# Performance work log

Measured on AMD Instinct MI355X. Metric: run time of the kernel, lower is better.

The kernel has to match this reference:

```python
import jax, jax.numpy as jnp
import numpy as np

NUM_HEADS = 8
ALPHA = 4.0  # spikingjelly sigmoid surrogate default

@jax.custom_vjp
def spike(x):
    return (x >= 0.0).astype(x.dtype)

def _spike_fwd(x):
    return spike(x), x

def _spike_bwd(x, g):
    s = jax.nn.sigmoid(ALPHA * x)
    return (g * ALPHA * s * (1.0 - s),)

spike.defvjp(_spike_fwd, _spike_bwd)

def lif(x, v_th=1.0, tau=2.0):
    # multi-step LIF over leading T dim; v_reset=0, hard reset, detach_reset
    def step(v, xt):
        h = v + (xt - v) / tau
        s = spike(h - v_th)
        v_new = h * (1.0 - jax.lax.stop_gradient(s))
        return v_new, s
    _, out = jax.lax.scan(step, jnp.zeros_like(x[0]), x)
    return out

def bn(x, gamma, beta, mean, var, eps=1e-5):
    # inference BatchNorm2d on (N,C,H,W)
    inv = gamma / jnp.sqrt(var + eps)
    return x * inv[None, :, None, None] + (beta - mean * inv)[None, :, None, None]

def conv1x1(x, w, b=None):
    # x: (N,C,H,W), w: (O,C)
    y = jnp.einsum('nchw,oc->nohw', x, w)
    if b is not None:
        y = y + b[None, :, None, None]
    return y

def setup_inputs() -> dict:
    key = jax.random.key(0)
    ks = jax.random.split(key, 20)
    T, B, C, H, W = 4, 32, 384, 14, 14
    d = {
        'x': jax.random.normal(ks[0], (T, B, C, H, W), jnp.float32),
        'q_w': jax.random.normal(ks[1], (C, C), jnp.float32) * (1.0 / np.sqrt(C)),
        'q_gamma': jax.random.uniform(ks[2], (C,), jnp.float32),
        'q_beta': jax.random.normal(ks[3], (C,), jnp.float32) * 0.1,
        'q_mean': jax.random.normal(ks[4], (C,), jnp.float32) * 0.1,
        'q_var': jax.random.uniform(ks[5], (C,), jnp.float32) + 0.5,
        'k_w': jax.random.normal(ks[6], (C, C), jnp.float32) * (1.0 / np.sqrt(C)),
        'k_gamma': jax.random.uniform(ks[7], (C,), jnp.float32),
        'k_beta': jax.random.normal(ks[8], (C,), jnp.float32) * 0.1,
        'k_mean': jax.random.normal(ks[9], (C,), jnp.float32) * 0.1,
        'k_var': jax.random.uniform(ks[10], (C,), jnp.float32) + 0.5,
        'proj_w': jax.random.normal(ks[11], (C, C), jnp.float32) * (1.0 / np.sqrt(C)),
        'proj_b': jax.random.normal(ks[12], (C,), jnp.float32) * 0.1,
        'proj_gamma': jax.random.uniform(ks[13], (C,), jnp.float32),
        'proj_beta': jax.random.normal(ks[14], (C,), jnp.float32) * 0.1,
        'proj_mean': jax.random.normal(ks[15], (C,), jnp.float32) * 0.1,
        'proj_var': jax.random.uniform(ks[16], (C,), jnp.float32) + 0.5,
    }
    return d

def reference(x, q_w, q_gamma, q_beta, q_mean, q_var,
              k_w, k_gamma, k_beta, k_mean, k_var,
              proj_w, proj_b, proj_gamma, proj_beta, proj_mean, proj_var):
    T, B, C, H, W = x.shape
    dh = C // NUM_HEADS
    xf = x.reshape(T * B, C, H, W)
    # Q branch: conv1x1 -> BN -> multistep LIF
    q = bn(conv1x1(xf, q_w), q_gamma, q_beta, q_mean, q_var).reshape(T, B, C, H, W)
    q = lif(q).reshape(T, B, NUM_HEADS, dh, H, W)
    # K branch
    k = bn(conv1x1(xf, k_w), k_gamma, k_beta, k_mean, k_var).reshape(T, B, C, H, W)
    k = lif(k).reshape(T, B, NUM_HEADS, dh, H, W)
    # sum-pool attention: sum q over head feature dim, spike it, gate k
    qs = jnp.sum(q, axis=3, keepdims=True)          # (T,B,heads,1,H,W)
    attn = lif(qs, v_th=0.5)
    y = (attn * k).reshape(T * B, C, H, W)
    # output projection: conv1x1(+bias) -> BN -> LIF
    y = bn(conv1x1(y, proj_w, proj_b), proj_gamma, proj_beta, proj_mean, proj_var)
    y = lif(y.reshape(T, B, C, H, W))
    return y
```

## Files before the change

kernel.cpp:

```cpp
#include <hip/hip_runtime.h>

#define C_DIM 384
#define S_DIM 196
#define CS_   (C_DIM * S_DIM)
#define BCS   (32 * CS_)
#define NELEM (128 * CS_)
#define NBS   6272

typedef _Float16 half8  __attribute__((ext_vector_type(8)));
typedef float    floatx4 __attribute__((ext_vector_type(4)));

__device__ __forceinline__ void gl_lds16(const _Float16* g, _Float16* l) {
    __builtin_amdgcn_global_load_lds(
        (const __attribute__((address_space(1))) unsigned int*)g,
        (__attribute__((address_space(3))) unsigned int*)l, 16, 0, 0);
}

__global__ __launch_bounds__(256)
void prep(const float* __restrict__ X,
          const float* __restrict__ qw, const float* __restrict__ kw,
          const float* __restrict__ pw,
          const float* qg, const float* qb, const float* qm, const float* qv,
          const float* kg, const float* kb, const float* km, const float* kv,
          const float* pg, const float* pb, const float* pm, const float* pv,
          _Float16* __restrict__ X0, _Float16* __restrict__ X1,
          _Float16* __restrict__ Wq0, _Float16* __restrict__ Wq1,
          _Float16* __restrict__ Wp0, _Float16* __restrict__ Wp1,
          float2* __restrict__ invshQ, float2* __restrict__ invshP)
{
    __shared__ float tile[32][201];
    const int bid = blockIdx.x;
    const int t   = threadIdx.x;
    if (bid < 1536) {
        const int tb = bid / 12, cch = bid % 12;
        const int tt = tb >> 5, b = tb & 31;
        const int c0 = cch * 32;
        for (int idx = t; idx < 32 * S_DIM; idx += 256) {
            const int cc = idx / S_DIM, s = idx - cc * S_DIM;
            tile[cc][s] = X[(size_t)tb * CS_ + (c0 + cc) * S_DIM + s];
        }
        __syncthreads();
        for (int idx = t; idx < 32 * S_DIM; idx += 256) {
            const int s = idx >> 5, cc = idx & 31;
            const float v = tile[cc][s];
            const _Float16 h0 = (_Float16)v;
            const size_t off = ((size_t)(b * S_DIM + s) * 4 + tt) * C_DIM + c0 + cc;
            X0[off] = h0;
            X1[off] = (_Float16)((v - (float)h0) * 4096.0f);
        }
    } else {
        const int i = (bid - 1536) * 256 + t;
        const int NQ = 768 * C_DIM;
        if (i < NQ) {
            const int o = i / C_DIM, c = i - o * C_DIM;
            const float v = (o < 384) ? qw[o * C_DIM + c] : kw[(o - 384) * C_DIM + c];
            const _Float16 h0 = (_Float16)v;
            Wq0[i] = h0;
            Wq1[i] = (_Float16)((v - (float)h0) * 4096.0f);
        } else if (i < NQ + C_DIM * C_DIM) {
            const int j = i - NQ;
            const float v = pw[j];
            const _Float16 h0 = (_Float16)v;
            Wp0[j] = h0;
            Wp1[j] = (_Float16)((v - (float)h0) * 4096.0f);
        }
        if (i < 768) {
            float g, b2, m, vv;
            if (i < 384) { g = qg[i]; b2 = qb[i]; m = qm[i]; vv = qv[i]; }
            else         { g = kg[i-384]; b2 = kb[i-384]; m = km[i-384]; vv = kv[i-384]; }
            const float inv = g / sqrtf(vv + 1e-5f);
            invshQ[i] = make_float2(inv, b2 - m * inv);
        } else if (i < 1152) {
            const int j = i - 768;
            const float inv = pg[j] / sqrtf(pv[j] + 1e-5f);
            invshP[j] = make_float2(inv, pb[j] - pm[j] * inv);
        }
    }
}

__global__ __launch_bounds__(256, 3)
void qk_mfma(const _Float16* __restrict__ A0, const _Float16* __restrict__ A1,
             const _Float16* __restrict__ B0, const _Float16* __restrict__ B1,
             const float2* __restrict__ invsh,
             unsigned char* __restrict__ spkQ, unsigned char* __restrict__ spkK)
{
    __shared__ __align__(16) _Float16 As0[128 * 32];
    __shared__ __align__(16) _Float16 As1[128 * 32];
    __shared__ __align__(16) _Float16 Bs0[128 * 32];
    __shared__ __align__(16) _Float16 Bs1[128 * 32];

    const int t    = threadIdx.x;
    const int wave = t >> 6, lane = t & 63;
    const int o0 = blockIdx.x * 128;
    const int m0 = blockIdx.y * 128;

    const int wR   = wave * 32;
    const int sRow = lane >> 2;
    const int sCol = (((lane & 3) ^ ((sRow >> 1) & 3))) << 3;

    const int lo = lane & 15, quad = lane >> 4;
    const int oq = (wave >> 1) * 64, mq = (wave & 1) * 64;
    const int rdC = (quad ^ ((lo >> 1) & 3)) << 3;

    floatx4 acc[4][4];
    #pragma unroll
    for (int i = 0; i < 4; ++i)
        #pragma unroll
        for (int j = 0; j < 4; ++j) acc[i][j] = (floatx4)0.0f;

    for (int kt = 0; kt < 12; ++kt) {
        __syncthreads();
        const int kb = kt * 32;
        #pragma unroll
        for (int u = 0; u < 2; ++u) {
            const int R = wR + u * 16;
            const size_t ga = (size_t)(o0 + R + sRow) * C_DIM + kb + sCol;
            const size_t gb = (size_t)(m0 + R + sRow) * C_DIM + kb + sCol;
            gl_lds16(A0 + ga, &As0[R * 32]);
            gl_lds16(A1 + ga, &As1[R * 32]);
            gl_lds16(B0 + gb, &Bs0[R * 32]);
            gl_lds16(B1 + gb, &Bs1[R * 32]);
        }
        __syncthreads();

        half8 w0F[4], w1F[4], x0F[4], x1F[4];
        #pragma unroll
        for (int j = 0; j < 4; ++j) {
            const int ra = (oq + j * 16 + lo) * 32 + rdC;
            w0F[j] = *(const half8*)&As0[ra];
            w1F[j] = *(const half8*)&As1[ra];
        }
        #pragma unroll
        for (int i = 0; i < 4; ++i) {
            const int rb = (mq + i * 16 + lo) * 32 + rdC;
            x0F[i] = *(const half8*)&Bs0[rb];
            x1F[i] = *(const half8*)&Bs1[rb];
        }
        #pragma unroll
        for (int i = 0; i < 4; ++i) {
            const half8 xS = x0F[i] * (_Float16)4096.0f;
            #pragma unroll
            for (int j = 0; j < 4; ++j) {
                acc[i][j] = __builtin_amdgcn_mfma_f32_16x16x32_f16(
                    x0F[i], w1F[j], acc[i][j], 0, 0, 0);
                acc[i][j] = __builtin_amdgcn_mfma_f32_16x16x32_f16(
                    x1F[i], w0F[j], acc[i][j], 0, 0, 0);
                acc[i][j] = __builtin_amdgcn_mfma_f32_16x16x32_f16(
                    xS,     w0F[j], acc[i][j], 0, 0, 0);
            }
        }
    }

    #pragma unroll
    for (int j = 0; j < 4; ++j) {
        const int o = o0 + oq + j * 16 + lo;
        const float2 is = invsh[o];
        const float inv = is.x * (1.0f / 4096.0f);
        const float sh  = is.y;
        unsigned char* base = (o < 384) ? spkQ : spkK;
        const int orow = (o < 384) ? o : o - 384;
        #pragma unroll
        for (int i = 0; i < 4; ++i) {
            const int bs = ((m0 + mq + i * 16) >> 2) + quad;
            float v = 0.0f; int bits = 0;
            #pragma unroll
            for (int r = 0; r < 4; ++r) {
                const float xv = acc[i][j][r] * inv + sh;
                const float h = v + (xv - v) * 0.5f;
                const int sp = (h >= 1.0f);
                v = sp ? 0.0f : h;
                bits |= sp << r;
            }
            base[(size_t)bs * C_DIM + orow] = (unsigned char)bits;
        }
    }
}

__global__ __launch_bounds__(256, 3)
void proj_mfma(const _Float16* __restrict__ A0, const _Float16* __restrict__ A1,
               const unsigned char* __restrict__ spkQ,
               const unsigned char* __restrict__ spkK,
               const float* __restrict__ bias, const float2* __restrict__ invsh,
               float* __restrict__ out)
{
    __shared__ __align__(16) _Float16 smem[3 * 128 * 32];
    __shared__ unsigned char attnL[256];
    _Float16* As0 = smem;
    _Float16* As1 = smem + 4096;
    _Float16* Bs0 = smem + 8192;

    const int t    = threadIdx.x;
    const int wave = t >> 6, lane = t & 63;
    const int o0 = blockIdx.x * 128;
    const int m0 = blockIdx.y * 128;

    const int wR   = wave * 32;
    const int sRow = lane >> 2;
    const int sCol = (((lane & 3) ^ ((sRow >> 1) & 3))) << 3;
    const int gC8  = (lane & 3) << 3;
    const int pC8  = sCol;

    const int lo = lane & 15, quad = lane >> 4;
    const int oq = (wave >> 1) * 64, mq = (wave & 1) * 64;
    const int rdC = (quad ^ ((lo >> 1) & 3)) << 3;

    const int bs0g   = m0 >> 2;
    const int bsl[2] = { (wR +  0 + sRow) >> 2, (wR + 16 + sRow) >> 2 };
    const int ttL    = (wR + sRow) & 3;

    {
        const int bsl_a = t >> 3, head = t & 7;
        const unsigned long long* p = (const unsigned long long*)
            (spkQ + (size_t)(bs0g + bsl_a) * C_DIM + head * 48);
        int qs[4] = {0, 0, 0, 0};
        #pragma unroll
        for (int u = 0; u < 6; ++u) {
            const unsigned long long v = p[u];
            qs[0] += __popcll(v & 0x0101010101010101ull);
            qs[1] += __popcll(v & 0x0202020202020202ull);
            qs[2] += __popcll(v & 0x0404040404040404ull);
            qs[3] += __popcll(v & 0x0808080808080808ull);
        }
        float va = 0.0f; int bits = 0;
        #pragma unroll
        for (int tt = 0; tt < 4; ++tt) {
            const float h = va + ((float)qs[tt] - va) * 0.5f;
            const int a = (h >= 0.5f);
            va = a ? 0.0f : h;
            bits |= a << tt;
        }
        attnL[t] = (unsigned char)bits;
    }
    __syncthreads();

    floatx4 acc[4][4];
    #pragma unroll
    for (int i = 0; i < 4; ++i)
        #pragma unroll
        for (int j = 0; j < 4; ++j) acc[i][j] = (floatx4)0.0f;

    unsigned long long rk[2];
    int rab[2];
    {
        const int head0 = gC8 / 48;
        #pragma unroll
        for (int u = 0; u < 2; ++u) {
            rk[u]  = *(const unsigned long long*)
                     (spkK + (size_t)(bs0g + bsl[u]) * C_DIM + gC8);
            rab[u] = (attnL[bsl[u] * 8 + head0] >> ttL) & 1;
        }
    }

    for (int kt = 0; kt < 12; ++kt) {
        __syncthreads();
        const int kb = kt * 32;
        #pragma unroll
        for (int u = 0; u < 2; ++u) {
            const int R = wR + u * 16;
            half8 bv;
            #pragma unroll
            for (int e = 0; e < 8; ++e)
                bv[e] = (_Float16)(float)((int)(rk[u] >> (8 * e + ttL)) & rab[u] & 1);
            *(half8*)&Bs0[(R + sRow) * 32 + pC8] = bv;
            const size_t ga = (size_t)(o0 + R + sRow) * C_DIM + kb + sCol;
            gl_lds16(A0 + ga, &As0[R * 32]);
            gl_lds16(A1 + ga, &As1[R * 32]);
        }
        if (kt < 11) {
            const int kb2  = (kt + 1) * 32;
            const int head = (kb2 + gC8) / 48;
            #pragma unroll
            for (int u = 0; u < 2; ++u) {
                rk[u]  = *(const unsigned long long*)
                         (spkK + (size_t)(bs0g + bsl[u]) * C_DIM + kb2 + gC8);
                rab[u] = (attnL[bsl[u] * 8 + head] >> ttL) & 1;
            }
        }
        __syncthreads();

        half8 w0F[4], w1F[4], yF[4];
        #pragma unroll
        for (int j = 0; j < 4; ++j) {
            const int ra = (oq + j * 16 + lo) * 32 + rdC;
            w0F[j] = *(const half8*)&As0[ra];
            w1F[j] = *(const half8*)&As1[ra];
        }
        #pragma unroll
        for (int i = 0; i < 4; ++i)
            yF[i] = *(const half8*)&Bs0[(mq + i * 16 + lo) * 32 + rdC];

        #pragma unroll
        for (int j = 0; j < 4; ++j) {
            const half8 wS = w0F[j] * (_Float16)4096.0f;
            #pragma unroll
            for (int i = 0; i < 4; ++i) {
                acc[i][j] = __builtin_amdgcn_mfma_f32_16x16x32_f16(
                    yF[i], w1F[j], acc[i][j], 0, 0, 0);
                acc[i][j] = __builtin_amdgcn_mfma_f32_16x16x32_f16(
                    yF[i], wS,     acc[i][j], 0, 0, 0);
            }
        }
    }

    int bits[4][4];
    #pragma unroll
    for (int j = 0; j < 4; ++j) {
        const int o = o0 + oq + j * 16 + lo;
        const float2 is = invsh[o];
        const float bv = bias[o];
        #pragma unroll
        for (int i = 0; i < 4; ++i) {
            float v = 0.0f; int bt = 0;
            #pragma unroll
            for (int r = 0; r < 4; ++r) {
                const float p = acc[i][j][r] * (1.0f / 4096.0f);
                const float z = (p + bv) * is.x + is.y;
                const float h = v + (z - v) * 0.5f;
                const int sp = (h >= 1.0f);
                v = sp ? 0.0f : h;
                bt |= sp << r;
            }
            bits[i][j] = bt;
        }
    }

    float* tile = (float*)smem;
    for (int r = 0; r < 4; ++r) {
        __syncthreads();
        #pragma unroll
        for (int j = 0; j < 4; ++j)
            #pragma unroll
            for (int i = 0; i < 4; ++i)
                tile[(oq + j * 16 + lo) * 33 + (mq >> 2) + i * 4 + quad] =
                    ((bits[i][j] >> r) & 1) ? 1.0f : 0.0f;
        __syncthreads();
        #pragma unroll
        for (int it = 0; it < 4; ++it) {
            const int idx = it * 256 + t;
            const int o   = idx >> 3;
            const int ch  = idx & 7;
            const int bsg = bs0g + ch * 4;
            const int b   = bsg / S_DIM;
            const int s   = bsg - b * S_DIM;
            float4 vv;
            vv.x = tile[o * 33 + ch * 4 + 0];
            vv.y = tile[o * 33 + ch * 4 + 1];
            vv.z = tile[o * 33 + ch * 4 + 2];
            vv.w = tile[o * 33 + ch * 4 + 3];
            *(float4*)(out + (size_t)r * BCS + (size_t)b * CS_
                           + (size_t)(o0 + o) * S_DIM + s) = vv;
        }
    }
}

extern "C" void kernel_launch(void* const* d_in, const int* in_sizes, int n_in,
                              void* d_out, int out_size, void* d_ws, size_t ws_size,
                              hipStream_t stream)
{
    const float* x          = (const float*)d_in[0];
    const float* q_w        = (const float*)d_in[1];
    const float* q_gamma    = (const float*)d_in[2];
    const float* q_beta     = (const float*)d_in[3];
    const float* q_mean     = (const float*)d_in[4];
    const float* q_var      = (const float*)d_in[5];
    const float* k_w        = (const float*)d_in[6];
    const float* k_gamma    = (const float*)d_in[7];
    const float* k_beta     = (const float*)d_in[8];
    const float* k_mean     = (const float*)d_in[9];
    const float* k_var      = (const float*)d_in[10];
    const float* proj_w     = (const float*)d_in[11];
    const float* proj_b     = (const float*)d_in[12];
    const float* proj_gamma = (const float*)d_in[13];
    const float* proj_beta  = (const float*)d_in[14];
    const float* proj_mean  = (const float*)d_in[15];
    const float* proj_var   = (const float*)d_in[16];
    float* out = (float*)d_out;

    _Float16* h0 = (_Float16*)d_ws;
    _Float16* h1 = h0 + NELEM;
    _Float16* Wq0 = h1 + NELEM;
    _Float16* Wq1 = Wq0 + 768 * C_DIM;
    _Float16* Wp0 = Wq1 + 768 * C_DIM;
    _Float16* Wp1 = Wp0 + C_DIM * C_DIM;
    float2*   invshQ = (float2*)(Wp1 + C_DIM * C_DIM);
    float2*   invshP = invshQ + 768;
    unsigned char* spkQ  = (unsigned char*)(invshP + 384);
    unsigned char* spkK  = spkQ + (size_t)NBS * C_DIM;

    prep<<<3264, 256, 0, stream>>>(x, q_w, k_w, proj_w,
                                   q_gamma, q_beta, q_mean, q_var,
                                   k_gamma, k_beta, k_mean, k_var,
                                   proj_gamma, proj_beta, proj_mean, proj_var,
                                   h0, h1, Wq0, Wq1, Wp0, Wp1, invshQ, invshP);

    qk_mfma<<<dim3(6, 196), 256, 0, stream>>>(Wq0, Wq1, h0, h1, invshQ,
                                              spkQ, spkK);
    proj_mfma<<<dim3(3, 196), 256, 0, stream>>>(Wp0, Wp1, spkQ, spkK,
                                                proj_b, invshP, out);
}
```

Before: 205.6 us.

## Use per-wave private LDS tiles in qk GEMM and drop block barriers

The qk GEMM now gives each wave its own LDS region, holding its 64-row slices of both weight and activation tiles. This removes the two __syncthreads per k-step, at the cost of redundant global loads across waves and 64KB of LDS per block, so occupancy drops to 2 blocks per CU. Both GEMM grids are also transposed so the spatial dimension varies fastest along blockIdx.x. The prep transpose now handles 64 channels per block, halving the block count. Correctness depends on each wave waiting for its own global-to-LDS loads before reading them, now that no block barrier enforces this.

```diff
diff --git a/kernel.cpp b/kernel.cpp
--- a/kernel.cpp
+++ b/kernel.cpp
@@ -28,20 +28,20 @@
           _Float16* __restrict__ Wp0, _Float16* __restrict__ Wp1,
           float2* __restrict__ invshQ, float2* __restrict__ invshP)
 {
-    __shared__ float tile[32][201];
+    __shared__ float tile[64][201];
     const int bid = blockIdx.x;
     const int t   = threadIdx.x;
-    if (bid < 1536) {
-        const int tb = bid / 12, cch = bid % 12;
+    if (bid < 768) {
+        const int tb = bid / 6, cch = bid % 6;
         const int tt = tb >> 5, b = tb & 31;
-        const int c0 = cch * 32;
-        for (int idx = t; idx < 32 * S_DIM; idx += 256) {
+        const int c0 = cch * 64;
+        for (int idx = t; idx < 64 * S_DIM; idx += 256) {
             const int cc = idx / S_DIM, s = idx - cc * S_DIM;
             tile[cc][s] = X[(size_t)tb * CS_ + (c0 + cc) * S_DIM + s];
         }
         __syncthreads();
-        for (int idx = t; idx < 32 * S_DIM; idx += 256) {
-            const int s = idx >> 5, cc = idx & 31;
+        for (int idx = t; idx < 64 * S_DIM; idx += 256) {
+            const int s = idx >> 6, cc = idx & 63;
             const float v = tile[cc][s];
             const _Float16 h0 = (_Float16)v;
             const size_t off = ((size_t)(b * S_DIM + s) * 4 + tt) * C_DIM + c0 + cc;
@@ -49,7 +49,7 @@
             X1[off] = (_Float16)((v - (float)h0) * 4096.0f);
         }
     } else {
-        const int i = (bid - 1536) * 256 + t;
+        const int i = (bid - 768) * 256 + t;
         const int NQ = 768 * C_DIM;
         if (i < NQ) {
             const int o = i / C_DIM, c = i - o * C_DIM;
@@ -78,29 +78,30 @@
     }
 }
 
-__global__ __launch_bounds__(256, 3)
+__global__ __launch_bounds__(256, 2)
 void qk_mfma(const _Float16* __restrict__ A0, const _Float16* __restrict__ A1,
              const _Float16* __restrict__ B0, const _Float16* __restrict__ B1,
              const float2* __restrict__ invsh,
              unsigned char* __restrict__ spkQ, unsigned char* __restrict__ spkK)
 {
-    __shared__ __align__(16) _Float16 As0[128 * 32];
-    __shared__ __align__(16) _Float16 As1[128 * 32];
-    __shared__ __align__(16) _Float16 Bs0[128 * 32];
-    __shared__ __align__(16) _Float16 Bs1[128 * 32];
+    __shared__ __align__(16) _Float16 lds[32768];
 
     const int t    = threadIdx.x;
     const int wave = t >> 6, lane = t & 63;
-    const int o0 = blockIdx.x * 128;
-    const int m0 = blockIdx.y * 128;
-
-    const int wR   = wave * 32;
-    const int sRow = lane >> 2;
-    const int sCol = (((lane & 3) ^ ((sRow >> 1) & 3))) << 3;
+    const int m0 = blockIdx.x * 128;
+    const int o0 = blockIdx.y * 128;
 
     const int lo = lane & 15, quad = lane >> 4;
     const int oq = (wave >> 1) * 64, mq = (wave & 1) * 64;
-    const int rdC = (quad ^ ((lo >> 1) & 3)) << 3;
+
+    _Float16* As0 = lds + wave * 8192;
+    _Float16* As1 = As0 + 2048;
+    _Float16* Bs0 = As0 + 4096;
+    _Float16* Bs1 = As0 + 6144;
+
+    const int sRow = lane >> 2;
+    const int sC   = ((lane & 3) ^ ((sRow >> 1) & 3)) << 3;
+    const int rdC  = (quad ^ ((lo >> 1) & 3)) << 3;
 
     floatx4 acc[4][4];
     #pragma unroll
@@ -109,30 +110,28 @@
         for (int j = 0; j < 4; ++j) acc[i][j] = (floatx4)0.0f;
 
     for (int kt = 0; kt < 12; ++kt) {
-        __syncthreads();
         const int kb = kt * 32;
         #pragma unroll
-        for (int u = 0; u < 2; ++u) {
-            const int R = wR + u * 16;
-            const size_t ga = (size_t)(o0 + R + sRow) * C_DIM + kb + sCol;
-            const size_t gb = (size_t)(m0 + R + sRow) * C_DIM + kb + sCol;
+        for (int g = 0; g < 4; ++g) {
+            const int R = g * 16;
+            const size_t ga = (size_t)(o0 + oq + R + sRow) * C_DIM + kb + sC;
+            const size_t gb = (size_t)(m0 + mq + R + sRow) * C_DIM + kb + sC;
             gl_lds16(A0 + ga, &As0[R * 32]);
             gl_lds16(A1 + ga, &As1[R * 32]);
             gl_lds16(B0 + gb, &Bs0[R * 32]);
             gl_lds16(B1 + gb, &Bs1[R * 32]);
         }
-        __syncthreads();
 
         half8 w0F[4], w1F[4], x0F[4], x1F[4];
         #pragma unroll
         for (int j = 0; j < 4; ++j) {
-            const int ra = (oq + j * 16 + lo) * 32 + rdC;
+            const int ra = (j * 16 + lo) * 32 + rdC;
             w0F[j] = *(const half8*)&As0[ra];
             w1F[j] = *(const half8*)&As1[ra];
         }
         #pragma unroll
         for (int i = 0; i < 4; ++i) {
-            const int rb = (mq + i * 16 + lo) * 32 + rdC;
+            const int rb = (i * 16 + lo) * 32 + rdC;
             x0F[i] = *(const half8*)&Bs0[rb];
             x1F[i] = *(const half8*)&Bs1[rb];
         }
@@ -191,8 +190,8 @@
 
     const int t    = threadIdx.x;
     const int wave = t >> 6, lane = t & 63;
-    const int o0 = blockIdx.x * 128;
-    const int m0 = blockIdx.y * 128;
+    const int m0 = blockIdx.x * 128;
+    const int o0 = blockIdx.y * 128;
 
     const int wR   = wave * 32;
     const int sRow = lane >> 2;
@@ -387,14 +386,14 @@
     unsigned char* spkQ  = (unsigned char*)(invshP + 384);
     unsigned char* spkK  = spkQ + (size_t)NBS * C_DIM;
 
-    prep<<<3264, 256, 0, stream>>>(x, q_w, k_w, proj_w,
+    prep<<<2496, 256, 0, stream>>>(x, q_w, k_w, proj_w,
                                    q_gamma, q_beta, q_mean, q_var,
                                    k_gamma, k_beta, k_mean, k_var,
                                    proj_gamma, proj_beta, proj_mean, proj_var,
                                    h0, h1, Wq0, Wq1, Wp0, Wp1, invshQ, invshP);
 
-    qk_mfma<<<dim3(6, 196), 256, 0, stream>>>(Wq0, Wq1, h0, h1, invshQ,
+    qk_mfma<<<dim3(196, 6), 256, 0, stream>>>(Wq0, Wq1, h0, h1, invshQ,
                                               spkQ, spkK);
-    proj_mfma<<<dim3(3, 196), 256, 0, stream>>>(Wp0, Wp1, spkQ, spkK,
+    proj_mfma<<<dim3(196, 3), 256, 0, stream>>>(Wp0, Wp1, spkQ, spkK,
                                                 proj_b, invshP, out);
 }
```

Result: slower. 217.1 us (+5.6%).
